# Performance work log

Measured on AMD Instinct MI355X. Metric: run time of the kernel, lower is better.

Reference implementation:

```python
import jax, jax.numpy as jnp
import numpy as np

HIDDEN = 2048
NUM_HEADS = 16
HEAD_DIM = 128
BLOCK_SIZE = 64
NUM_ACTIVE_BLOCKS = 4  # diagonal pattern -> bandwidth = 2 blocks each side
NEG_INF = -1e30  # stand-in for -inf that is safe under softmax in fp32


def _block_diagonal_additive_mask(seq_len: int) -> jnp.ndarray:
    """Token-level additive mask [S, S]; 0 where block |bi-bj|<=bandwidth, -inf else."""
    bandwidth = NUM_ACTIVE_BLOCKS // 2
    bid = jnp.arange(seq_len) // BLOCK_SIZE  # [S]
    active = jnp.abs(bid[:, None] - bid[None, :]) <= bandwidth  # [S, S] bool
    return jnp.where(active, 0.0, NEG_INF).astype(jnp.float32)


def setup_inputs() -> dict:
    key = jax.random.key(0)
    k0, k1, k2, k3, k4 = jax.random.split(key, 5)
    B, S = 2, 2048
    scale = 1.0 / np.sqrt(HIDDEN)
    return {
        "hidden_states": jax.random.normal(k0, (B, S, HIDDEN), dtype=jnp.float32),
        "Wq": jax.random.normal(k1, (HIDDEN, NUM_HEADS * HEAD_DIM), dtype=jnp.float32) * scale,
        "Wk": jax.random.normal(k2, (HIDDEN, NUM_HEADS * HEAD_DIM), dtype=jnp.float32) * scale,
        "Wv": jax.random.normal(k3, (HIDDEN, NUM_HEADS * HEAD_DIM), dtype=jnp.float32) * scale,
        "Wo": jax.random.normal(k4, (NUM_HEADS * HEAD_DIM, HIDDEN), dtype=jnp.float32) * scale,
    }


def reference(hidden_states, Wq, Wk, Wv, Wo):
    B, S, _ = hidden_states.shape
    scaling = HEAD_DIM ** -0.5

    # projections -> [B, H, S, D]
    def split_heads(x):
        return x.reshape(B, S, NUM_HEADS, HEAD_DIM).transpose(0, 2, 1, 3)

    q = split_heads(hidden_states @ Wq)
    k = split_heads(hidden_states @ Wk)
    v = split_heads(hidden_states @ Wv)

    mask = _block_diagonal_additive_mask(S)  # [S, S]

    # scores [B, H, S, S]
    scores = jnp.einsum("bhsd,bhtd->bhst", q, k) * scaling + mask[None, None]
    attn = jax.nn.softmax(scores.astype(jnp.float32), axis=-1).astype(q.dtype)

    out = jnp.einsum("bhst,bhtd->bhsd", attn, v)  # [B, H, S, D]
    out = out.transpose(0, 2, 1, 3).reshape(B, S, NUM_HEADS * HEAD_DIM)
    return out @ Wo
```

## Files before the change

### kernel.cpp

```cpp
#include <hip/hip_runtime.h>

typedef __attribute__((ext_vector_type(4))) float f32x4;
typedef __attribute__((ext_vector_type(16))) float f32x16;
typedef __attribute__((ext_vector_type(8))) _Float16 f16x8;
typedef __attribute__((ext_vector_type(4))) _Float16 f16x4;

__device__ __forceinline__ void gload_lds16(const void* g, void* l) {
  __builtin_amdgcn_global_load_lds((__attribute__((address_space(1))) void*)(g),
                                   (__attribute__((address_space(3))) void*)(l), 16, 0, 0);
}

__global__ __launch_bounds__(256) void prep(const float* __restrict__ Hs,
                                            const float* __restrict__ W0, const float* __restrict__ W1,
                                            const float* __restrict__ W2, const float* __restrict__ W3,
                                            _Float16* __restrict__ Hb, _Float16* __restrict__ Wt) {
  __shared__ _Float16 tile[64][65];
  const int bid = blockIdx.x, tid = threadIdx.x;
  if (bid < 8192) {
    int i = (bid * 256 + tid) * 4;
    float4 v = *(const float4*)(Hs + i);
    f16x4 o = { (_Float16)v.x, (_Float16)v.y, (_Float16)v.z, (_Float16)v.w };
    *(f16x4*)(Hb + i) = o;
    return;
  }
  const int t = bid - 8192;
  const int z = t >> 10, k0 = ((t >> 5) & 31) * 64, n0 = (t & 31) * 64;
  const float* W = z == 0 ? W0 : z == 1 ? W1 : z == 2 ? W2 : W3;
  _Float16* Wo_ = Wt + (size_t)z * (2048u * 2048u);
  #pragma unroll
  for (int p = 0; p < 4; ++p) {
    int o = p * 256 + tid, r = o >> 4, c = o & 15;
    float4 v = *(const float4*)(W + (size_t)(k0 + r) * 2048 + n0 + c * 4);
    tile[r][c * 4 + 0] = (_Float16)v.x;
    tile[r][c * 4 + 1] = (_Float16)v.y;
    tile[r][c * 4 + 2] = (_Float16)v.z;
    tile[r][c * 4 + 3] = (_Float16)v.w;
  }
  __syncthreads();
  #pragma unroll
  for (int p = 0; p < 2; ++p) {
    int o = p * 256 + tid, nl = o >> 3, c = o & 7;
    f16x8 u;
    #pragma unroll
    for (int i = 0; i < 8; ++i) u[i] = tile[c * 8 + i][nl];
    *(f16x8*)(Wo_ + (size_t)(n0 + nl) * 2048 + k0 + c * 8) = u;
  }
}

template <int SM, int SN, typename OutT>
__device__ __forceinline__ void gemm_tile(const _Float16* __restrict__ A,
                                          const _Float16* __restrict__ Bt,
                                          OutT* __restrict__ C,
                                          int K, int N, int m0, int n0, _Float16* S) {
  _Float16* As = S;
  _Float16* Bs = S + SM * 64 * 64;
  const int tid = threadIdx.x;
  const int lane = tid & 63, w = tid >> 6, l32 = lane & 31, half = lane >> 5;
  const int wm = (w & 1) * SM * 32, wn = (w >> 1) * SN * 32;
  f32x16 acc[SM][SN];
  #pragma unroll
  for (int s = 0; s < SM; ++s)
    #pragma unroll
    for (int t = 0; t < SN; ++t) acc[s][t] = 0;

  for (int k0 = 0; k0 < K; k0 += 64) {
    __syncthreads();
    #pragma unroll
    for (int p = 0; p < SM * 2; ++p) {
      int o = p * 256 + tid, r = o >> 3, c = o & 7;
      gload_lds16(A + (size_t)(m0 + r) * K + k0 + ((c ^ (r & 7)) * 8), (char*)As + o * 16);
    }
    #pragma unroll
    for (int p = 0; p < SN * 2; ++p) {
      int o = p * 256 + tid, r = o >> 3, c = o & 7;
      gload_lds16(Bt + (size_t)(n0 + r) * K + k0 + ((c ^ (r & 7)) * 8), (char*)Bs + o * 16);
    }
    __builtin_amdgcn_s_waitcnt(0);
    __syncthreads();
    #pragma unroll
    for (int kk = 0; kk < 4; ++kk) {
      const int slot = ((2 * kk + half) ^ (l32 & 7)) * 8;
      f16x8 af[SM], bf[SN];
      #pragma unroll
      for (int s = 0; s < SM; ++s) af[s] = *(const f16x8*)(As + (wm + s * 32 + l32) * 64 + slot);
      #pragma unroll
      for (int t = 0; t < SN; ++t) bf[t] = *(const f16x8*)(Bs + (wn + t * 32 + l32) * 64 + slot);
      #pragma unroll
      for (int s = 0; s < SM; ++s)
        #pragma unroll
        for (int t = 0; t < SN; ++t)
          acc[s][t] = __builtin_amdgcn_mfma_f32_32x32x16_f16(bf[t], af[s], acc[s][t], 0, 0, 0);
    }
  }
  #pragma unroll
  for (int s = 0; s < SM; ++s) {
    const size_t row = (size_t)(m0 + wm + s * 32 + l32);
    #pragma unroll
    for (int t = 0; t < SN; ++t) {
      #pragma unroll
      for (int g = 0; g < 4; ++g) {
        const int col = n0 + wn + t * 32 + g * 8 + 4 * half;
        if constexpr (sizeof(OutT) == 2) {
          f16x4 o = { (_Float16)acc[s][t][4 * g + 0], (_Float16)acc[s][t][4 * g + 1],
                      (_Float16)acc[s][t][4 * g + 2], (_Float16)acc[s][t][4 * g + 3] };
          *(f16x4*)((_Float16*)C + row * N + col) = o;
        } else {
          f32x4 o = { acc[s][t][4 * g + 0], acc[s][t][4 * g + 1],
                      acc[s][t][4 * g + 2], acc[s][t][4 * g + 3] };
          *(f32x4*)((float*)C + row * N + col) = o;
        }
      }
    }
  }
}

__global__ __launch_bounds__(256, 2) void qkvv(const _Float16* __restrict__ Hb,
                                               const _Float16* __restrict__ Wt,
                                               _Float16* __restrict__ Qb,
                                               _Float16* __restrict__ Vtb) {
  __shared__ _Float16 S[24576];
  const int id = blockIdx.x;
  if (id < 512) {
    const int z = id >> 8, t = id & 255;
    gemm_tile<4, 2>(Hb, Wt + (size_t)z * 4194304, Qb + (size_t)z * 8388608,
                    2048, 2048, (t >> 4) * 256, (t & 15) * 128, S);
  } else {
    const int t = id - 512;
    gemm_tile<2, 4>(Wt + (size_t)2 * 4194304, Hb, Vtb,
                    2048, 4096, (t >> 4) * 128, (t & 15) * 256, S);
  }
}

__global__ __launch_bounds__(256) void gemm_wo(const _Float16* __restrict__ A,
                                               const _Float16* __restrict__ Bt,
                                               float* __restrict__ C) {
  __shared__ _Float16 S[16384];
  const int t = blockIdx.x;
  gemm_tile<2, 2>(A, Bt, C, 2048, 2048, (t >> 4) * 128, (t & 15) * 128, S);
}

__global__ __launch_bounds__(256) void attn(const _Float16* __restrict__ Qg,
                                            const _Float16* __restrict__ Kg,
                                            const _Float16* __restrict__ Vtg,
                                            _Float16* __restrict__ Og) {
  const int t = blockIdx.x, h = blockIdx.y, b = blockIdx.z;
  __shared__ _Float16 Qs[128 * 128];
  __shared__ _Float16 Ks[64 * 128];
  __shared__ _Float16 Vs[128 * 64];
  const int tid = threadIdx.x;
  const int lane = tid & 63, w = tid >> 6, l16 = lane & 15, quad = lane >> 4;
  const int qbw = 2 * t + (w >> 1);
  const char* QsB = (const char*)Qs;
  const char* KsB = (const char*)Ks;
  const char* VsB = (const char*)Vs;

  #pragma unroll
  for (int p = 0; p < 8; ++p) {
    int o = p * 256 + tid, r = o >> 4, c = o & 15;
    gload_lds16(Qg + (size_t)(b * 2048 + t * 128 + r) * 2048 + h * 128 + ((c ^ (r & 15)) * 8),
                (char*)Qs + o * 16);
  }
  __builtin_amdgcn_s_waitcnt(0);
  __syncthreads();
  f16x8 qf[2][4];
  #pragma unroll
  for (int qc = 0; qc < 2; ++qc)
    #pragma unroll
    for (int ks = 0; ks < 4; ++ks)
      qf[qc][ks] = *(const f16x8*)(QsB + (w * 32 + qc * 16 + l16) * 256 +
                                   (((ks * 4 + quad) ^ l16) * 16));

  const float scale = 0.08838834764831845f;
  float m_[2] = {-1e30f, -1e30f}, l_[2] = {0.f, 0.f};
  f32x4 oacc[8][2];
  #pragma unroll
  for (int dt = 0; dt < 8; ++dt)
    #pragma unroll
    for (int qc = 0; qc < 2; ++qc) oacc[dt][qc] = (f32x4){0.f, 0.f, 0.f, 0.f};

  for (int jj = 0; jj < 6; ++jj) {
    const int j = 2 * t - 2 + jj;
    const int jc = j < 0 ? 0 : (j > 31 ? 31 : j);
    __syncthreads();
    #pragma unroll
    for (int p = 0; p < 4; ++p) {
      int o = p * 256 + tid, r = o >> 4, c = o & 15;
      gload_lds16(Kg + (size_t)(b * 2048 + jc * 64 + r) * 2048 + h * 128 + ((c ^ (r & 15)) * 8),
                  (char*)Ks + o * 16);
    }
    #pragma unroll
    for (int p = 0; p < 4; ++p) {
      int o = p * 256 + tid, d = o >> 3, c = o & 7;
      gload_lds16(Vtg + (size_t)(h * 128 + d) * 4096 + b * 2048 + jc * 64 + ((c ^ (d & 7)) * 8),
                  (char*)Vs + o * 16);
    }
    __builtin_amdgcn_s_waitcnt(0);
    __syncthreads();

    const bool valid = (j >= 0) && (j <= 31) && (j >= qbw - 2) && (j <= qbw + 2);
    if (valid) {
      f32x4 sc[4][2];
      #pragma unroll
      for (int kt = 0; kt < 4; ++kt)
        #pragma unroll
        for (int qc = 0; qc < 2; ++qc) sc[kt][qc] = (f32x4){0.f, 0.f, 0.f, 0.f};
      #pragma unroll
      for (int kt = 0; kt < 4; ++kt)
        #pragma unroll
        for (int ks = 0; ks < 4; ++ks) {
          f16x8 kf = *(const f16x8*)(KsB + (kt * 16 + l16) * 256 + (((ks * 4 + quad) ^ l16) * 16));
          #pragma unroll
          for (int qc = 0; qc < 2; ++qc)
            sc[kt][qc] = __builtin_amdgcn_mfma_f32_16x16x32_f16(kf, qf[qc][ks], sc[kt][qc], 0, 0, 0);
        }
      #pragma unroll
      for (int qc = 0; qc < 2; ++qc) {
        float mj = -1e30f;
        #pragma unroll
        for (int kt = 0; kt < 4; ++kt)
          #pragma unroll
          for (int r = 0; r < 4; ++r) {
            float v = sc[kt][qc][r] * scale;
            sc[kt][qc][r] = v;
            mj = fmaxf(mj, v);
          }
        mj = fmaxf(mj, __shfl_xor(mj, 16));
        mj = fmaxf(mj, __shfl_xor(mj, 32));
        const float mn = fmaxf(m_[qc], mj);
        const float alpha = __expf(m_[qc] - mn);
        float s_ = 0.f;
        #pragma unroll
        for (int kt = 0; kt < 4; ++kt)
          #pragma unroll
          for (int r = 0; r < 4; ++r) {
            float p = __expf(sc[kt][qc][r] - mn);
            sc[kt][qc][r] = p;
            s_ += p;
          }
        s_ += __shfl_xor(s_, 16);
        s_ += __shfl_xor(s_, 32);
        l_[qc] = l_[qc] * alpha + s_;
        m_[qc] = mn;
        #pragma unroll
        for (int dt = 0; dt < 8; ++dt) oacc[dt][qc] *= alpha;
      }
      #pragma unroll
      for (int kt = 0; kt < 4; ++kt) {
        f16x4 pb[2];
        #pragma unroll
        for (int qc = 0; qc < 2; ++qc)
          pb[qc] = (f16x4){ (_Float16)sc[kt][qc][0], (_Float16)sc[kt][qc][1],
                            (_Float16)sc[kt][qc][2], (_Float16)sc[kt][qc][3] };
        #pragma unroll
        for (int dt = 0; dt < 8; ++dt) {
          f16x4 vv = *(const f16x4*)(VsB + (dt * 16 + l16) * 128 +
                                     (((2 * kt + (quad >> 1)) ^ (l16 & 7)) * 16) + (quad & 1) * 8);
          #pragma unroll
          for (int qc = 0; qc < 2; ++qc)
            oacc[dt][qc] = __builtin_amdgcn_mfma_f32_16x16x16f16(vv, pb[qc], oacc[dt][qc], 0, 0, 0);
        }
      }
    }
  }

  #pragma unroll
  for (int qc = 0; qc < 2; ++qc) {
    const float pinv = 1.0f / l_[qc];
    const size_t orow = (size_t)(b * 2048 + t * 128 + w * 32 + qc * 16 + l16);
    #pragma unroll
    for (int dt = 0; dt < 8; ++dt) {
      f16x4 ov = { (_Float16)(oacc[dt][qc][0] * pinv), (_Float16)(oacc[dt][qc][1] * pinv),
                   (_Float16)(oacc[dt][qc][2] * pinv), (_Float16)(oacc[dt][qc][3] * pinv) };
      *(f16x4*)(Og + orow * 2048 + h * 128 + dt * 16 + quad * 4) = ov;
    }
  }
}

extern "C" void kernel_launch(void* const* d_in, const int* in_sizes, int n_in,
                              void* d_out, int out_size, void* d_ws, size_t ws_size,
                              hipStream_t stream) {
  const float* Hs = (const float*)d_in[0];
  const float* Wq = (const float*)d_in[1];
  const float* Wk = (const float*)d_in[2];
  const float* Wv = (const float*)d_in[3];
  const float* Wo = (const float*)d_in[4];
  _Float16* Hb  = (_Float16*)d_ws;
  _Float16* Wt  = Hb  + 8388608;
  _Float16* Qb  = Wt  + 16777216;
  _Float16* Kb  = Qb  + 8388608;
  _Float16* Vtb = Kb  + 8388608;
  _Float16* Ob  = Vtb + 8388608;
  float* out = (float*)d_out;
  (void)Kb;

  prep<<<12288, 256, 0, stream>>>(Hs, Wq, Wk, Wv, Wo, Hb, Wt);
  qkvv<<<768, 256, 0, stream>>>(Hb, Wt, Qb, Vtb);
  attn<<<dim3(16, 16, 2), 256, 0, stream>>>(Qb, Kb, Vtb, Ob);
  gemm_wo<<<512, 256, 0, stream>>>(Ob, Wt + (size_t)3 * 4194304, out);
}
```

Measured before the change: 355.2 us.

## Replace QKV projection with 256x256-tile 8-wave ping-pong pipelined GEMM

Replaces the QKV projection kernel with a new GEMM using 256x256 output tiles, 512 threads and double-buffered LDS filled by direct global-to-LDS loads. The K loop is software-pipelined: fragment loads, async staging of later tiles and MFMA bursts are interleaved with sched_barriers, explicit vmcnt waits and setprio. The larger tile raises arithmetic intensity and is meant to hide global load latency. In exchange it uses 128KB of LDS per block and only 384 blocks, which leaves an uneven last wave across CUs.

```diff
diff --git a/kernel.cpp b/kernel.cpp
--- a/kernel.cpp
+++ b/kernel.cpp
@@ -9,6 +9,10 @@
   __builtin_amdgcn_global_load_lds((__attribute__((address_space(1))) void*)(g),
                                    (__attribute__((address_space(3))) void*)(l), 16, 0, 0);
 }
+
+#define SB0() __builtin_amdgcn_sched_barrier(0)
+#define WAITV6() asm volatile("s_waitcnt vmcnt(6)" ::: "memory")
+#define WAITV0() asm volatile("s_waitcnt vmcnt(0)" ::: "memory")
 
 __global__ __launch_bounds__(256) void prep(const float* __restrict__ Hs,
                                             const float* __restrict__ W0, const float* __restrict__ W1,
@@ -114,20 +118,129 @@
   }
 }
 
-__global__ __launch_bounds__(256, 2) void qkvv(const _Float16* __restrict__ Hb,
-                                               const _Float16* __restrict__ Wt,
-                                               _Float16* __restrict__ Qb,
-                                               _Float16* __restrict__ Vtb) {
-  __shared__ _Float16 S[24576];
+__device__ __forceinline__ void gemm256(const _Float16* __restrict__ A,
+                                        const _Float16* __restrict__ Bt,
+                                        _Float16* __restrict__ C, int ldc,
+                                        int m0, int n0, _Float16* S) {
+  _Float16* const As0 = S;
+  _Float16* const As1 = S + 16384;
+  _Float16* const Bs0 = S + 32768;
+  _Float16* const Bs1 = S + 49152;
+  const int tid = (int)threadIdx.x;
+  const int lane = tid & 63, w = tid >> 6, l32 = lane & 31, half = lane >> 5;
+  const int wm = (w & 1) * 128, wn = (w >> 1) * 64;
+
+  f32x16 acc[4][2];
+  #pragma unroll
+  for (int s = 0; s < 4; ++s)
+    #pragma unroll
+    for (int t = 0; t < 2; ++t) acc[s][t] = 0;
+
+  f16x8 af[2][4];
+  f16x8 bf[2][4];
+
+  auto stageA = [&](_Float16* dst, int ar, int kt) {
+    const int r = tid >> 3, c = tid & 7;
+    gload_lds16(A + (size_t)(m0 + ar + r) * 2048 + kt * 64 + ((c ^ (r & 7)) << 3),
+                (char*)dst + ar * 128 + tid * 16);
+  };
+  auto stageB = [&](_Float16* dst, int br, int kt) {
+    const int r = tid >> 3, c = tid & 7;
+    gload_lds16(Bt + (size_t)(n0 + br + r) * 2048 + kt * 64 + ((c ^ (r & 7)) << 3),
+                (char*)dst + br * 128 + tid * 16);
+  };
+  auto ldA = [&](const _Float16* as, int p) {
+    #pragma unroll
+    for (int s2 = 0; s2 < 2; ++s2)
+      #pragma unroll
+      for (int kk = 0; kk < 4; ++kk)
+        af[s2][kk] = *(const f16x8*)(as + (wm + p * 64 + s2 * 32 + l32) * 64 +
+                                     (((2 * kk + half) ^ (l32 & 7)) << 3));
+  };
+  auto ldB = [&](const _Float16* bs, int q) {
+    #pragma unroll
+    for (int kk = 0; kk < 4; ++kk)
+      bf[q][kk] = *(const f16x8*)(bs + (wn + q * 32 + l32) * 64 +
+                                  (((2 * kk + half) ^ (l32 & 7)) << 3));
+  };
+  auto mm = [&](int sp, int q) {
+    __builtin_amdgcn_s_setprio(1);
+    #pragma unroll
+    for (int kk = 0; kk < 4; ++kk)
+      #pragma unroll
+      for (int s2 = 0; s2 < 2; ++s2)
+        acc[sp * 2 + s2][q] = __builtin_amdgcn_mfma_f32_32x32x16_f16(
+            bf[q][kk], af[s2][kk], acc[sp * 2 + s2][q], 0, 0, 0);
+    __builtin_amdgcn_s_setprio(0);
+  };
+
+  auto tile = [&](int kt, _Float16* Ac, _Float16* Bc, _Float16* An, _Float16* Bn) {
+    const bool g1 = (kt + 1) < 32, g2 = (kt + 2) < 32;
+    ldA(Ac, 0); ldB(Bc, 0);
+    if (g1) { stageA(An, 64, kt + 1); stageA(An, 192, kt + 1); }
+    SB0(); __builtin_amdgcn_s_barrier(); SB0();
+    mm(0, 0);
+    SB0(); __builtin_amdgcn_s_barrier(); SB0();
+    ldB(Bc, 1);
+    if (g2) { stageA(Ac, 0, kt + 2); stageA(Ac, 128, kt + 2); }
+    SB0(); __builtin_amdgcn_s_barrier(); SB0();
+    mm(0, 1);
+    SB0(); __builtin_amdgcn_s_barrier(); SB0();
+    ldA(Ac, 1);
+    if (g2) { stageB(Bc, 0, kt + 2); stageB(Bc, 64, kt + 2); }
+    SB0(); __builtin_amdgcn_s_barrier(); SB0();
+    mm(1, 1);
+    SB0(); __builtin_amdgcn_s_barrier(); SB0();
+    if (g2) { stageB(Bc, 128, kt + 2); stageB(Bc, 192, kt + 2); }
+    if (g2) { WAITV6(); } else { WAITV0(); }
+    SB0(); __builtin_amdgcn_s_barrier(); SB0();
+    mm(1, 0);
+    SB0(); __builtin_amdgcn_s_barrier(); SB0();
+  };
+
+  stageA(As0, 0, 0); stageA(As0, 64, 0); stageA(As0, 128, 0); stageA(As0, 192, 0);
+  stageB(Bs0, 0, 0); stageB(Bs0, 64, 0); stageB(Bs0, 128, 0); stageB(Bs0, 192, 0);
+  stageA(As1, 0, 1); stageA(As1, 128, 1);
+  stageB(Bs1, 0, 1); stageB(Bs1, 64, 1); stageB(Bs1, 128, 1); stageB(Bs1, 192, 1);
+  WAITV6();
+  SB0(); __builtin_amdgcn_s_barrier(); SB0();
+
+  #pragma unroll 1
+  for (int kt = 0; kt < 32; kt += 2) {
+    tile(kt, As0, Bs0, As1, Bs1);
+    tile(kt + 1, As1, Bs1, As0, Bs0);
+  }
+
+  #pragma unroll
+  for (int s = 0; s < 4; ++s) {
+    const size_t row = (size_t)(wm + s * 32 + l32);
+    #pragma unroll
+    for (int t = 0; t < 2; ++t)
+      #pragma unroll
+      for (int g = 0; g < 4; ++g) {
+        const int col = wn + t * 32 + g * 8 + 4 * half;
+        f16x4 o = { (_Float16)acc[s][t][4 * g + 0], (_Float16)acc[s][t][4 * g + 1],
+                    (_Float16)acc[s][t][4 * g + 2], (_Float16)acc[s][t][4 * g + 3] };
+        *(f16x4*)(C + row * ldc + col) = o;
+      }
+  }
+}
+
+__global__ __launch_bounds__(512, 2) void qkvv8(const _Float16* __restrict__ Hb,
+                                                const _Float16* __restrict__ Wt,
+                                                _Float16* __restrict__ Qb,
+                                                _Float16* __restrict__ Kb,
+                                                _Float16* __restrict__ Vtb) {
+  __shared__ _Float16 S[65536];
   const int id = blockIdx.x;
-  if (id < 512) {
-    const int z = id >> 8, t = id & 255;
-    gemm_tile<4, 2>(Hb, Wt + (size_t)z * 4194304, Qb + (size_t)z * 8388608,
-                    2048, 2048, (t >> 4) * 256, (t & 15) * 128, S);
+  if (id < 256) {
+    const int m0 = (id >> 4) * 256, n0 = (id & 15) * 256;
+    _Float16* C = (n0 < 2048 ? Qb + n0 : Kb + (n0 - 2048)) + (size_t)m0 * 2048;
+    gemm256(Hb, Wt, C, 2048, m0, n0, S);
   } else {
-    const int t = id - 512;
-    gemm_tile<2, 4>(Wt + (size_t)2 * 4194304, Hb, Vtb,
-                    2048, 4096, (t >> 4) * 128, (t & 15) * 256, S);
+    const int t = id - 256;
+    const int m0 = (t >> 4) * 256, n0 = (t & 15) * 256;
+    gemm256(Wt + (size_t)2 * 4194304, Hb, Vtb + (size_t)m0 * 4096 + n0, 4096, m0, n0, S);
   }
 }
 
@@ -291,10 +404,9 @@
   _Float16* Vtb = Kb  + 8388608;
   _Float16* Ob  = Vtb + 8388608;
   float* out = (float*)d_out;
-  (void)Kb;
 
   prep<<<12288, 256, 0, stream>>>(Hs, Wq, Wk, Wv, Wo, Hb, Wt);
-  qkvv<<<768, 256, 0, stream>>>(Hb, Wt, Qb, Vtb);
+  qkvv8<<<384, 512, 0, stream>>>(Hb, Wt, Qb, Kb, Vtb);
   attn<<<dim3(16, 16, 2), 256, 0, stream>>>(Qb, Kb, Vtb, Ob);
   gemm_wo<<<512, 256, 0, stream>>>(Ob, Wt + (size_t)3 * 4194304, out);
 }
```

New measurement: 361.9 us. Within noise of the previous version (+1.9%).
